# Kernel optimization log

Hardware: AMD Instinct MI355X
Metric: run time of the kernel (lower is better)

## Reference

```python
import jax, jax.numpy as jnp
import numpy as np

L, B, H, R = 128, 4, 768, 97
LN_EPS = 1e-5


def setup_inputs() -> dict:
    key = jax.random.key(0)
    ks = jax.random.split(key, 8)
    s = 0.02
    return {
        "h_re1": jax.random.normal(ks[0], (L, B, H), jnp.float32),
        "h_re2": jax.random.normal(ks[1], (L, B, H), jnp.float32),
        "mask": jax.random.uniform(ks[2], (L, B), jnp.float32),
        "Wr": jax.random.normal(ks[3], (H, 2 * H), jnp.float32) * s,
        "br": jnp.zeros((H,), jnp.float32),
        "Wh": jax.random.normal(ks[4], (H, 3 * H), jnp.float32) * s,
        "bh": jnp.zeros((H,), jnp.float32),
        "gamma": jnp.ones((H,), jnp.float32),
        "beta": jnp.zeros((H,), jnp.float32),
        "Wo": jax.random.normal(ks[5], (R, H), jnp.float32) * s,
        "bo": jnp.zeros((R,), jnp.float32),
    }


def reference(h_re1, h_re2, mask, Wr, br, Wh, bh, gamma, beta, Wo, bo):
    # h_re1, h_re2: [L, B, H]; mask: [L, B]
    h = h_re2.shape[-1]
    # global context: tanh(Linear(cat(h_re1,h_re2))), max over length -> [B, H]
    g = jnp.tanh(jnp.einsum('lbi,hi->lbh', jnp.concatenate([h_re1, h_re2], axis=-1), Wr) + br)
    g = jnp.max(g, axis=0)  # [B, H]
    # hid2hid(cat(r1, r2, g)) == r1 @ W1.T + r2 @ W2.T + g @ W3.T + b
    # (avoids materializing the [L,L,B,3H] repeat+cat tensor)
    W1, W2, W3 = Wh[:, :h], Wh[:, h:2 * h], Wh[:, 2 * h:]
    a = jnp.einsum('lbi,hi->lbh', h_re2, W1)          # varies over first pair axis
    b2 = jnp.einsum('lbi,hi->lbh', h_re2, W2)         # varies over second pair axis
    gp = jnp.einsum('bi,hi->bh', g, W3) + bh          # constant over pairs
    pre = a[:, None, :, :] + b2[None, :, :, :] + gp   # [L, L, B, H]
    # LayerNorm over last dim (biased variance, as in torch)
    mu = jnp.mean(pre, axis=-1, keepdims=True)
    var = jnp.var(pre, axis=-1, keepdims=True)
    x = (pre - mu) * jax.lax.rsqrt(var + LN_EPS) * gamma + beta
    x = jax.nn.elu(x)  # dropout is identity in eval mode
    out = jax.nn.sigmoid(jnp.einsum('klbh,rh->klbr', x, Wo) + bo)  # [L, L, B, R]
    # pairwise mask: mask_e1 * mask_e2, broadcast over relation dim
    m = mask[:, None, :, None] * mask[None, :, :, None]
    return out * m
```

## Files before the change

### kernel.cpp

```cpp
#include <hip/hip_runtime.h>
#include <hip/hip_bf16.h>
#include <stdint.h>

#define L_ 128
#define B_ 4
#define H_ 768
#define R_ 97
#define LN_EPS 1e-5f

typedef _Float16 f16x8 __attribute__((ext_vector_type(8)));
typedef _Float16 f16x4 __attribute__((ext_vector_type(4)));
typedef _Float16 f16x2 __attribute__((ext_vector_type(2)));
typedef float f32x4 __attribute__((ext_vector_type(4)));

extern "C" __device__ _Float16 __ocml_exp2_f16(_Float16);

__device__ inline f16x8 cvt8(float4 v0, float4 v1) {
  f16x8 o;
  o[0] = (_Float16)v0.x; o[1] = (_Float16)v0.y; o[2] = (_Float16)v0.z; o[3] = (_Float16)v0.w;
  o[4] = (_Float16)v1.x; o[5] = (_Float16)v1.y; o[6] = (_Float16)v1.z; o[7] = (_Float16)v1.w;
  return o;
}

__global__ __launch_bounds__(256) void prep_all(const float* __restrict__ h1,
                                                const float* __restrict__ h2,
                                                const float* __restrict__ Wr,
                                                const float* __restrict__ Wh,
                                                const float* __restrict__ Wo,
                                                const float* __restrict__ gamma,
                                                const float* __restrict__ beta,
                                                _Float16* __restrict__ ccH,
                                                _Float16* __restrict__ BpR,
                                                _Float16* __restrict__ BpW,
                                                _Float16* __restrict__ WoP,
                                                _Float16* __restrict__ gbH,
                                                unsigned int* __restrict__ gmaxU) {
  int blk = blockIdx.x;
  if (blk < 512) {
    const float2* s1 = (const float2*)(h1 + (size_t)blk * H_);
    const float2* s2 = (const float2*)(h2 + (size_t)blk * H_);
    f16x2* d = (f16x2*)(ccH + (size_t)blk * (2 * H_));
    for (int i = threadIdx.x; i < H_ / 2; i += 256) {
      float2 v = s1[i]; f16x2 o; o[0] = (_Float16)v.x; o[1] = (_Float16)v.y; d[i] = o;
    }
    for (int i = threadIdx.x; i < H_ / 2; i += 256) {
      float2 v = s2[i]; f16x2 o; o[0] = (_Float16)v.x; o[1] = (_Float16)v.y; d[H_ / 2 + i] = o;
    }
    return;
  }
  blk -= 512;
  if (blk < 576) {
    int c = blk * 256 + threadIdx.x;
    int l = c & 63, u = c >> 6;
    int nt = u % 48, ks = u / 48;
    int n = nt * 16 + (l & 15);
    int k = ks * 32 + ((l >> 4) << 3);
    const float4* s = (const float4*)(Wr + (size_t)n * 1536 + k);
    *(f16x8*)(BpR + (size_t)c * 8) = cvt8(s[0], s[1]);
    return;
  }
  blk -= 576;
  if (blk < 576) {
    int c = blk * 256 + threadIdx.x;
    int l = c & 63, u = c >> 6;
    int nt = u % 96, ks = u / 96;
    int n = nt * 16 + (l & 15);
    int k = ks * 32 + ((l >> 4) << 3);
    const float* src = (n < 768) ? (Wh + (size_t)n * 2304 + k)
                                 : (Wh + (size_t)(n - 768) * 2304 + 768 + k);
    const float4* s = (const float4*)src;
    *(f16x8*)(BpW + (size_t)c * 8) = cvt8(s[0], s[1]);
    return;
  }
  blk -= 576;
  if (blk < 48) {
    int c = blk * 256 + threadIdx.x;
    int l = c & 63, u = c >> 6;
    int nt = u & 7, ks = u >> 3;
    int n = nt * 16 + (l & 15);
    int k = ks * 32 + ((l >> 4) << 3);
    f16x8 o = {};
    if (n < R_) {
      const float4* s = (const float4*)(Wo + (size_t)n * 768 + k);
      o = cvt8(s[0], s[1]);
    }
    *(f16x8*)(WoP + (size_t)c * 8) = o;
    return;
  }
  blk -= 48;
  if (blk < 3) {
    int i = blk * 256 + threadIdx.x;
    if (i < H_) {
      gbH[i] = (_Float16)gamma[i];
      gbH[H_ + i] = (_Float16)beta[i];
    }
    return;
  }
  blk -= 3;
  int i = blk * 256 + threadIdx.x;
  if (i < B_ * H_) gmaxU[i] = 0u;
}

__device__ __forceinline__ void gemm_g_tile(int nb, int mb,
                                            const _Float16* __restrict__ A,
                                            const _Float16* __restrict__ BpR,
                                            const float* __restrict__ br,
                                            unsigned int* __restrict__ gmaxU) {
  int w = threadIdx.x >> 6, l = threadIdx.x & 63;
  int row0 = mb * 32 + (w & 1) * 16;
  int nt0 = nb * 4 + (w >> 1) * 2;
  const f16x8* ap = (const f16x8*)(A + (size_t)(row0 + (l & 15)) * 1536 + (l >> 4) * 8);
  const f16x8* bp = (const f16x8*)(BpR + ((size_t)nt0 * 64 + l) * 8);
  f32x4 acc0 = {}, acc1 = {};
  f16x8 ac = ap[0], b0c = bp[0], b1c = bp[64];
  for (int ks = 0; ks < 48; ++ks) {
    f16x8 an = {}, b0n = {}, b1n = {};
    if (ks < 47) {
      an = ap[(ks + 1) * 4];
      b0n = bp[(size_t)(ks + 1) * 3072];
      b1n = bp[(size_t)(ks + 1) * 3072 + 64];
    }
    acc0 = __builtin_amdgcn_mfma_f32_16x16x32_f16(ac, b0c, acc0, 0, 0, 0);
    acc1 = __builtin_amdgcn_mfma_f32_16x16x32_f16(ac, b1c, acc1, 0, 0, 0);
    ac = an; b0c = b0n; b1c = b1n;
  }
#pragma unroll
  for (int q = 0; q < 2; ++q) {
    f32x4 acc = q ? acc1 : acc0;
    int col = nb * 64 + (w >> 1) * 32 + q * 16 + (l & 15);
#pragma unroll
    for (int r = 0; r < 4; ++r) {
      int row = row0 + (l >> 4) * 4 + r;
      float t = tanhf(acc[r] + br[col]) + 1.0f;
      atomicMax(&gmaxU[(row & 3) * H_ + col], __float_as_uint(t));
    }
  }
}

__device__ __forceinline__ void gemm_ab_tile(int nb, int mb,
                                             const _Float16* __restrict__ ccH,
                                             const _Float16* __restrict__ BpW,
                                             _Float16* __restrict__ aH,
                                             _Float16* __restrict__ bH) {
  int w = threadIdx.x >> 6, l = threadIdx.x & 63;
  int row0 = mb * 32 + (w & 1) * 16;
  int nt0 = nb * 4 + (w >> 1) * 2;
  const f16x8* ap = (const f16x8*)(ccH + (size_t)(row0 + (l & 15)) * 1536 + 768 + (l >> 4) * 8);
  const f16x8* bp = (const f16x8*)(BpW + ((size_t)nt0 * 64 + l) * 8);
  f32x4 acc0 = {}, acc1 = {};
  f16x8 ac = ap[0], b0c = bp[0], b1c = bp[64];
  for (int ks = 0; ks < 24; ++ks) {
    f16x8 an = {}, b0n = {}, b1n = {};
    if (ks < 23) {
      an = ap[(ks + 1) * 4];
      b0n = bp[(size_t)(ks + 1) * 6144];
      b1n = bp[(size_t)(ks + 1) * 6144 + 64];
    }
    acc0 = __builtin_amdgcn_mfma_f32_16x16x32_f16(ac, b0c, acc0, 0, 0, 0);
    acc1 = __builtin_amdgcn_mfma_f32_16x16x32_f16(ac, b1c, acc1, 0, 0, 0);
    ac = an; b0c = b0n; b1c = b1n;
  }
#pragma unroll
  for (int q = 0; q < 2; ++q) {
    f32x4 acc = q ? acc1 : acc0;
    int col = nb * 64 + (w >> 1) * 32 + q * 16 + (l & 15);
#pragma unroll
    for (int r = 0; r < 4; ++r) {
      int row = row0 + (l >> 4) * 4 + r;
      float v = acc[r];
      if (col < 768) aH[(size_t)row * H_ + col] = (_Float16)v;
      else           bH[(size_t)row * H_ + (col - 768)] = (_Float16)v;
    }
  }
}

__global__ __launch_bounds__(256) void gemm_both(const _Float16* __restrict__ ccH,
                                                 const _Float16* __restrict__ BpR,
                                                 const _Float16* __restrict__ BpW,
                                                 const float* __restrict__ br,
                                                 unsigned int* __restrict__ gmaxU,
                                                 _Float16* __restrict__ aH,
                                                 _Float16* __restrict__ bH) {
  int bid = blockIdx.x;
  if (bid < 192) {
    gemm_g_tile(bid % 12, bid / 12, ccH, BpR, br, gmaxU);
  } else {
    int j2 = bid - 192;
    gemm_ab_tile(j2 % 24, j2 / 24, ccH, BpW, aH, bH);
  }
}

__global__ __launch_bounds__(256) void gp_kernel(const float* __restrict__ Wh,
                                                 const unsigned int* __restrict__ gmaxU,
                                                 const float* __restrict__ bh,
                                                 float* __restrict__ gpv) {
  int n = blockIdx.x;
  int w = threadIdx.x >> 6, l = threadIdx.x & 63;
  const float* wr = Wh + (size_t)n * 2304 + 1536;
  const unsigned int* gm = gmaxU + (size_t)w * H_;
  float s = 0.f;
#pragma unroll
  for (int t = 0; t < 12; ++t) {
    int i = l + 64 * t;
    s += wr[i] * (__uint_as_float(gm[i]) - 1.0f);
  }
#pragma unroll
  for (int off = 32; off; off >>= 1) s += __shfl_xor(s, off);
  if (l == 0) gpv[(size_t)w * H_ + n] = s + bh[n];
}

__global__ __launch_bounds__(256) void stats(const _Float16* __restrict__ aH,
                                             const _Float16* __restrict__ bH,
                                             const float* __restrict__ gpv,
                                             _Float16* __restrict__ aH2,
                                             float* __restrict__ S,
                                             float* __restrict__ Q) {
  int r = blockIdx.x * 4 + (threadIdx.x >> 6);
  int l = threadIdx.x & 63;
  float s = 0.f, q = 0.f;
  if (r < 512) {
    int b = r & 3;
    const f16x4* ap = (const f16x4*)(aH + (size_t)r * H_);
    const float4* gp4 = (const float4*)(gpv + (size_t)b * H_);
    f16x4* op = (f16x4*)(aH2 + (size_t)r * H_);
#pragma unroll
    for (int t = 0; t < 3; ++t) {
      int i = t * 64 + l;
      f16x4 av = ap[i];
      float4 g4 = gp4[i];
      f16x4 o;
      o[0] = (_Float16)((float)av[0] + g4.x);
      o[1] = (_Float16)((float)av[1] + g4.y);
      o[2] = (_Float16)((float)av[2] + g4.z);
      o[3] = (_Float16)((float)av[3] + g4.w);
      op[i] = o;
#pragma unroll
      for (int j = 0; j < 4; ++j) { float y = (float)o[j]; s += y; q += y * y; }
    }
  } else {
    const f16x4* bp = (const f16x4*)(bH + (size_t)(r - 512) * H_);
#pragma unroll
    for (int t = 0; t < 3; ++t) {
      f16x4 bv = bp[t * 64 + l];
#pragma unroll
      for (int j = 0; j < 4; ++j) { float y = (float)bv[j]; s += y; q += y * y; }
    }
  }
#pragma unroll
  for (int off = 32; off; off >>= 1) {
    s += __shfl_xor(s, off);
    q += __shfl_xor(q, off);
  }
  if (l == 0) { S[r] = s; Q[r] = q; }
}

__global__ __launch_bounds__(256) void dotab(const _Float16* __restrict__ aH2,
                                             const _Float16* __restrict__ bH,
                                             const float* __restrict__ S,
                                             const float* __restrict__ Q,
                                             float* __restrict__ mu_arr,
                                             float* __restrict__ rs_arr) {
  int w = threadIdx.x >> 6, l = threadIdx.x & 63;
  int ltq = blockIdx.x, kt = blockIdx.y, b = blockIdx.z;
  int lt = ltq * 4 + w;
  const f16x8* ap = (const f16x8*)(aH2 + ((size_t)(kt * 16 + (l & 15)) * 4 + b) * H_ + (l >> 4) * 8);
  const f16x8* bp = (const f16x8*)(bH + ((size_t)(lt * 16 + (l & 15)) * 4 + b) * H_ + (l >> 4) * 8);
  f32x4 acc = {};
  f16x8 a0 = ap[0], b0 = bp[0], a1 = ap[4], b1 = bp[4];
  for (int ks = 0; ks < 24; ++ks) {
    f16x8 a2 = {}, b2 = {};
    if (ks < 22) { a2 = ap[(ks + 2) * 4]; b2 = bp[(ks + 2) * 4]; }
    acc = __builtin_amdgcn_mfma_f32_16x16x32_f16(a0, b0, acc, 0, 0, 0);
    a0 = a1; b0 = b1; a1 = a2; b1 = b2;
  }
#pragma unroll
  for (int r = 0; r < 4; ++r) {
    int k = kt * 16 + (l >> 4) * 4 + r;
    int lg = lt * 16 + (l & 15);
    int arow = k * 4 + b, brow = lg * 4 + b;
    float mu = (S[arow] + S[512 + brow]) * (1.f / H_);
    float q2 = Q[arow] + Q[512 + brow] + 2.f * acc[r];
    float var = fmaxf(q2 * (1.f / H_) - mu * mu, 0.f);
    float rs = rsqrtf(var + LN_EPS);
    size_t idx = (size_t)k * 512 + (size_t)lg * 4 + b;
    mu_arr[idx] = mu;
    rs_arr[idx] = rs;
  }
}

__global__ __launch_bounds__(256) void fused2(const _Float16* __restrict__ aH2,
                                              const _Float16* __restrict__ bH,
                                              const _Float16* __restrict__ gbH,
                                              const _Float16* __restrict__ WoP,
                                              const float* __restrict__ bo,
                                              const float* __restrict__ mask,
                                              const float* __restrict__ mu_arr,
                                              const float* __restrict__ rs_arr,
                                              float* __restrict__ out) {
  __shared__ __align__(16) _Float16 WoLds[3][4096];
  int tid = threadIdx.x, w = tid >> 6, l = tid & 63;
  int m0 = blockIdx.x * 64;
  int myrow = m0 + w * 16 + (l & 15);
  int b = myrow & 3, li = (myrow >> 2) & 127, kk = myrow >> 9;
  const f16x8* ap = (const f16x8*)(aH2 + ((size_t)kk * 4 + b) * H_ + (l >> 4) * 8);
  const f16x8* bp = (const f16x8*)(bH + ((size_t)li * 4 + b) * H_ + (l >> 4) * 8);
  const f16x8* gp8 = (const f16x8*)(gbH + (l >> 4) * 8);
  const f16x8* be8 = (const f16x8*)(gbH + H_ + (l >> 4) * 8);
  float mu = mu_arr[myrow], rs = rs_arr[myrow];
  _Float16 muh = (_Float16)mu, rsh = (_Float16)rs;
  _Float16 l2e = (_Float16)1.44269504f;
  f16x8 mu8, rs8, zero8, one8, l2e8;
#pragma unroll
  for (int j = 0; j < 8; ++j) {
    mu8[j] = muh; rs8[j] = rsh;
    zero8[j] = (_Float16)0.f; one8[j] = (_Float16)1.f; l2e8[j] = l2e;
  }

  const uint4* wog = (const uint4*)WoP;
  {
    uint4* d0 = (uint4*)&WoLds[0][0];
    uint4* d1 = (uint4*)&WoLds[1][0];
    d0[tid] = wog[tid];            d0[256 + tid] = wog[256 + tid];
    d1[tid] = wog[512 + tid];      d1[256 + tid] = wog[512 + 256 + tid];
  }
  __syncthreads();

  f16x8 a8 = ap[0], b8 = bp[0], g8 = gp8[0], e8 = be8[0];

  int cur = 0, wt = 2;
  f32x4 acc[7] = {};
  for (int ks = 0; ks < 24; ++ks) {
    uint4 wo0 = {}, wo1 = {};
    f16x8 an = {}, bn = {}, gn = {}, en = {};
    if (ks < 22) {
      wo0 = wog[(ks + 2) * 512 + tid];
      wo1 = wog[(ks + 2) * 512 + 256 + tid];
    }
    if (ks < 23) {
      an = ap[(ks + 1) * 4];
      bn = bp[(ks + 1) * 4];
      gn = gp8[(ks + 1) * 4];
      en = be8[(ks + 1) * 4];
    }
    f16x8 x = a8 + b8;
    f16x8 c1 = rs8 * g8;
    f16x8 yv = (x - mu8) * c1 + e8;
    f16x8 y2 = yv * l2e8;
    f16x8 ex;
#pragma unroll
    for (int j = 0; j < 8; ++j) ex[j] = __ocml_exp2_f16(y2[j]);
    ex = ex - one8;
    f16x8 av = __builtin_elementwise_max(yv, zero8) + __builtin_elementwise_min(ex, zero8);
    __syncthreads();
    if (ks < 22) {
      uint4* d = (uint4*)&WoLds[wt][0];
      d[tid] = wo0;
      d[256 + tid] = wo1;
    }
    const f16x8* bvp = (const f16x8*)&WoLds[cur][0];
#pragma unroll
    for (int q = 0; q < 7; ++q) {
      f16x8 bv = bvp[q * 64 + l];
      acc[q] = __builtin_amdgcn_mfma_f32_16x16x32_f16(av, bv, acc[q], 0, 0, 0);
    }
    a8 = an; b8 = bn; g8 = gn; e8 = en;
    cur = (cur == 2) ? 0 : cur + 1;
    wt = (wt == 2) ? 0 : wt + 1;
  }
  float mv[4];
#pragma unroll
  for (int r = 0; r < 4; ++r) {
    int row = m0 + w * 16 + (l >> 4) * 4 + r;
    int bb = row & 3, ll = (row >> 2) & 127, kx = row >> 9;
    mv[r] = mask[kx * 4 + bb] * mask[ll * 4 + bb];
  }
#pragma unroll
  for (int q = 0; q < 7; ++q) {
    int col = q * 16 + (l & 15);
    if (col < R_) {
      float bov = bo[col];
#pragma unroll
      for (int r = 0; r < 4; ++r) {
        int row = m0 + w * 16 + (l >> 4) * 4 + r;
        float z = acc[q][r] + bov;
        out[(size_t)row * R_ + col] = mv[r] / (1.f + __expf(-z));
      }
    }
  }
}

extern "C" void kernel_launch(void* const* d_in, const int* in_sizes, int n_in,
                              void* d_out, int out_size, void* d_ws, size_t ws_size,
                              hipStream_t stream) {
  const float* h1    = (const float*)d_in[0];
  const float* h2    = (const float*)d_in[1];
  const float* mask  = (const float*)d_in[2];
  const float* Wr    = (const float*)d_in[3];
  const float* br    = (const float*)d_in[4];
  const float* Wh    = (const float*)d_in[5];
  const float* bh    = (const float*)d_in[6];
  const float* gamma = (const float*)d_in[7];
  const float* beta  = (const float*)d_in[8];
  const float* Wo    = (const float*)d_in[9];
  const float* bo    = (const float*)d_in[10];
  float* out = (float*)d_out;
  char* ws = (char*)d_ws;

  _Float16* ccH = (_Float16*)ws;                    size_t off = 512 * 1536 * 2;
  _Float16* BpR = (_Float16*)(ws + off);            off += (size_t)1536 * 768 * 2;
  _Float16* BpW = (_Float16*)(ws + off);            off += (size_t)768 * 1536 * 2;
  _Float16* WoP = (_Float16*)(ws + off);            off += 768 * 128 * 2;
  _Float16* gbH = (_Float16*)(ws + off);            off += 4096;
  _Float16* aH  = (_Float16*)(ws + off);            off += 512 * 768 * 2;
  _Float16* bH  = (_Float16*)(ws + off);            off += 512 * 768 * 2;
  _Float16* aH2 = (_Float16*)(ws + off);            off += 512 * 768 * 2;
  unsigned int* gmaxU = (unsigned int*)(ws + off);  off += 3072 * 4;
  float* gpv = (float*)(ws + off);                  off += 3072 * 4;
  float* S   = (float*)(ws + off);                  off += 1024 * 4;
  float* Q   = (float*)(ws + off);                  off += 1024 * 4;
  float* mu_arr = (float*)(ws + off);               off += 65536 * 4;
  float* rs_arr = (float*)(ws + off);               off += 65536 * 4;

  prep_all<<<512 + 576 + 576 + 48 + 3 + 12, 256, 0, stream>>>(h1, h2, Wr, Wh, Wo, gamma, beta,
                                                              ccH, BpR, BpW, WoP, gbH, gmaxU);

  gemm_both<<<576, 256, 0, stream>>>(ccH, BpR, BpW, br, gmaxU, aH, bH);
  gp_kernel<<<768, 256, 0, stream>>>(Wh, gmaxU, bh, gpv);
  stats<<<256, 256, 0, stream>>>(aH, bH, gpv, aH2, S, Q);
  dotab<<<dim3(2, 8, 4), 256, 0, stream>>>(aH2, bH, S, Q, mu_arr, rs_arr);

  fused2<<<1024, 256, 0, stream>>>(aH2, bH, gbH, WoP, bo, mask, mu_arr, rs_arr, out);
}
```

Measured before the change: 92.51 us.

## Fuse fp32-to-fp16 input conversion into GEMM loads and restage Wo tiles in LDS

The GEMMs now read fp32 h1/h2/Wr/Wh directly and convert them to fp16 in registers, so the separate pre-pass that wrote converted and packed copies of those tensors (and its workspace traffic) is gone. This trades a write and reread of about 5 MB of fp16 for reading fp32 operands inside the GEMM, where the loads are now strided rows rather than the old packed layout. The fused2 kernel also changes from a 3-slot rotating Wo prefetch to three phases that each bulk-load 8 k-steps of Wo into a larger shared buffer. That adds barriers and removes the overlap between loads and compute.

Result: slower. 142.8 us (+54.4%).

```diff
diff --git a/kernel.cpp b/kernel.cpp
--- a/kernel.cpp
+++ b/kernel.cpp
@@ -22,57 +22,13 @@
   return o;
 }
 
-__global__ __launch_bounds__(256) void prep_all(const float* __restrict__ h1,
-                                                const float* __restrict__ h2,
-                                                const float* __restrict__ Wr,
-                                                const float* __restrict__ Wh,
-                                                const float* __restrict__ Wo,
+__global__ __launch_bounds__(256) void prep_all(const float* __restrict__ Wo,
                                                 const float* __restrict__ gamma,
                                                 const float* __restrict__ beta,
-                                                _Float16* __restrict__ ccH,
-                                                _Float16* __restrict__ BpR,
-                                                _Float16* __restrict__ BpW,
                                                 _Float16* __restrict__ WoP,
                                                 _Float16* __restrict__ gbH,
                                                 unsigned int* __restrict__ gmaxU) {
   int blk = blockIdx.x;
-  if (blk < 512) {
-    const float2* s1 = (const float2*)(h1 + (size_t)blk * H_);
-    const float2* s2 = (const float2*)(h2 + (size_t)blk * H_);
-    f16x2* d = (f16x2*)(ccH + (size_t)blk * (2 * H_));
-    for (int i = threadIdx.x; i < H_ / 2; i += 256) {
-      float2 v = s1[i]; f16x2 o; o[0] = (_Float16)v.x; o[1] = (_Float16)v.y; d[i] = o;
-    }
-    for (int i = threadIdx.x; i < H_ / 2; i += 256) {
-      float2 v = s2[i]; f16x2 o; o[0] = (_Float16)v.x; o[1] = (_Float16)v.y; d[H_ / 2 + i] = o;
-    }
-    return;
-  }
-  blk -= 512;
-  if (blk < 576) {
-    int c = blk * 256 + threadIdx.x;
-    int l = c & 63, u = c >> 6;
-    int nt = u % 48, ks = u / 48;
-    int n = nt * 16 + (l & 15);
-    int k = ks * 32 + ((l >> 4) << 3);
-    const float4* s = (const float4*)(Wr + (size_t)n * 1536 + k);
-    *(f16x8*)(BpR + (size_t)c * 8) = cvt8(s[0], s[1]);
-    return;
-  }
-  blk -= 576;
-  if (blk < 576) {
-    int c = blk * 256 + threadIdx.x;
-    int l = c & 63, u = c >> 6;
-    int nt = u % 96, ks = u / 96;
-    int n = nt * 16 + (l & 15);
-    int k = ks * 32 + ((l >> 4) << 3);
-    const float* src = (n < 768) ? (Wh + (size_t)n * 2304 + k)
-                                 : (Wh + (size_t)(n - 768) * 2304 + 768 + k);
-    const float4* s = (const float4*)src;
-    *(f16x8*)(BpW + (size_t)c * 8) = cvt8(s[0], s[1]);
-    return;
-  }
-  blk -= 576;
   if (blk < 48) {
     int c = blk * 256 + threadIdx.x;
     int l = c & 63, u = c >> 6;
@@ -102,91 +58,99 @@
 }
 
 __device__ __forceinline__ void gemm_g_tile(int nb, int mb,
-                                            const _Float16* __restrict__ A,
-                                            const _Float16* __restrict__ BpR,
+                                            const float* __restrict__ h1,
+                                            const float* __restrict__ h2,
+                                            const float* __restrict__ Wr,
                                             const float* __restrict__ br,
                                             unsigned int* __restrict__ gmaxU) {
   int w = threadIdx.x >> 6, l = threadIdx.x & 63;
   int row0 = mb * 32 + (w & 1) * 16;
   int nt0 = nb * 4 + (w >> 1) * 2;
-  const f16x8* ap = (const f16x8*)(A + (size_t)(row0 + (l & 15)) * 1536 + (l >> 4) * 8);
-  const f16x8* bp = (const f16x8*)(BpR + ((size_t)nt0 * 64 + l) * 8);
+  int r = row0 + (l & 15);
+  int kbase = (l >> 4) * 8;
+  const float4* a1p = (const float4*)(h1 + (size_t)r * H_ + kbase);
+  const float4* a2p = (const float4*)(h2 + (size_t)r * H_ + kbase);
+  const float4* b0p = (const float4*)(Wr + (size_t)(nt0 * 16 + (l & 15)) * 1536 + kbase);
+  const float4* b1p = (const float4*)(Wr + (size_t)((nt0 + 1) * 16 + (l & 15)) * 1536 + kbase);
   f32x4 acc0 = {}, acc1 = {};
-  f16x8 ac = ap[0], b0c = bp[0], b1c = bp[64];
+#pragma unroll 4
   for (int ks = 0; ks < 48; ++ks) {
-    f16x8 an = {}, b0n = {}, b1n = {};
-    if (ks < 47) {
-      an = ap[(ks + 1) * 4];
-      b0n = bp[(size_t)(ks + 1) * 3072];
-      b1n = bp[(size_t)(ks + 1) * 3072 + 64];
-    }
-    acc0 = __builtin_amdgcn_mfma_f32_16x16x32_f16(ac, b0c, acc0, 0, 0, 0);
-    acc1 = __builtin_amdgcn_mfma_f32_16x16x32_f16(ac, b1c, acc1, 0, 0, 0);
-    ac = an; b0c = b0n; b1c = b1n;
+    const float4* asrc = (ks < 24) ? (a1p + ks * 8) : (a2p + (ks - 24) * 8);
+    f16x8 av = cvt8(asrc[0], asrc[1]);
+    f16x8 b0 = cvt8(b0p[ks * 8], b0p[ks * 8 + 1]);
+    f16x8 b1 = cvt8(b1p[ks * 8], b1p[ks * 8 + 1]);
+    acc0 = __builtin_amdgcn_mfma_f32_16x16x32_f16(av, b0, acc0, 0, 0, 0);
+    acc1 = __builtin_amdgcn_mfma_f32_16x16x32_f16(av, b1, acc1, 0, 0, 0);
   }
 #pragma unroll
   for (int q = 0; q < 2; ++q) {
     f32x4 acc = q ? acc1 : acc0;
-    int col = nb * 64 + (w >> 1) * 32 + q * 16 + (l & 15);
-#pragma unroll
-    for (int r = 0; r < 4; ++r) {
-      int row = row0 + (l >> 4) * 4 + r;
-      float t = tanhf(acc[r] + br[col]) + 1.0f;
+    int col = (nt0 + q) * 16 + (l & 15);
+#pragma unroll
+    for (int rr = 0; rr < 4; ++rr) {
+      int row = row0 + (l >> 4) * 4 + rr;
+      float t = tanhf(acc[rr] + br[col]) + 1.0f;
       atomicMax(&gmaxU[(row & 3) * H_ + col], __float_as_uint(t));
     }
   }
 }
 
 __device__ __forceinline__ void gemm_ab_tile(int nb, int mb,
-                                             const _Float16* __restrict__ ccH,
-                                             const _Float16* __restrict__ BpW,
+                                             const float* __restrict__ h2,
+                                             const float* __restrict__ Wh,
                                              _Float16* __restrict__ aH,
                                              _Float16* __restrict__ bH) {
   int w = threadIdx.x >> 6, l = threadIdx.x & 63;
   int row0 = mb * 32 + (w & 1) * 16;
   int nt0 = nb * 4 + (w >> 1) * 2;
-  const f16x8* ap = (const f16x8*)(ccH + (size_t)(row0 + (l & 15)) * 1536 + 768 + (l >> 4) * 8);
-  const f16x8* bp = (const f16x8*)(BpW + ((size_t)nt0 * 64 + l) * 8);
+  int r = row0 + (l & 15);
+  int kbase = (l >> 4) * 8;
+  const float4* ap = (const float4*)(h2 + (size_t)r * H_ + kbase);
+  int n0 = nt0 * 16 + (l & 15);
+  int n1 = n0 + 16;
+  const float* b0s = (n0 < 768) ? (Wh + (size_t)n0 * 2304 + kbase)
+                                : (Wh + (size_t)(n0 - 768) * 2304 + 768 + kbase);
+  const float* b1s = (n1 < 768) ? (Wh + (size_t)n1 * 2304 + kbase)
+                                : (Wh + (size_t)(n1 - 768) * 2304 + 768 + kbase);
+  const float4* b0p = (const float4*)b0s;
+  const float4* b1p = (const float4*)b1s;
   f32x4 acc0 = {}, acc1 = {};
-  f16x8 ac = ap[0], b0c = bp[0], b1c = bp[64];
+#pragma unroll 4
   for (int ks = 0; ks < 24; ++ks) {
-    f16x8 an = {}, b0n = {}, b1n = {};
-    if (ks < 23) {
-      an = ap[(ks + 1) * 4];
-      b0n = bp[(size_t)(ks + 1) * 6144];
-      b1n = bp[(size_t)(ks + 1) * 6144 + 64];
-    }
-    acc0 = __builtin_amdgcn_mfma_f32_16x16x32_f16(ac, b0c, acc0, 0, 0, 0);
-    acc1 = __builtin_amdgcn_mfma_f32_16x16x32_f16(ac, b1c, acc1, 0, 0, 0);
-    ac = an; b0c = b0n; b1c = b1n;
+    f16x8 av = cvt8(ap[ks * 8], ap[ks * 8 + 1]);
+    f16x8 b0 = cvt8(b0p[ks * 8], b0p[ks * 8 + 1]);
+    f16x8 b1 = cvt8(b1p[ks * 8], b1p[ks * 8 + 1]);
+    acc0 = __builtin_amdgcn_mfma_f32_16x16x32_f16(av, b0, acc0, 0, 0, 0);
+    acc1 = __builtin_amdgcn_mfma_f32_16x16x32_f16(av, b1, acc1, 0, 0, 0);
   }
 #pragma unroll
   for (int q = 0; q < 2; ++q) {
     f32x4 acc = q ? acc1 : acc0;
-    int col = nb * 64 + (w >> 1) * 32 + q * 16 + (l & 15);
-#pragma unroll
-    for (int r = 0; r < 4; ++r) {
-      int row = row0 + (l >> 4) * 4 + r;
-      float v = acc[r];
+    int col = (nt0 + q) * 16 + (l & 15);
+#pragma unroll
+    for (int rr = 0; rr < 4; ++rr) {
+      int row = row0 + (l >> 4) * 4 + rr;
+      float v = acc[rr];
       if (col < 768) aH[(size_t)row * H_ + col] = (_Float16)v;
       else           bH[(size_t)row * H_ + (col - 768)] = (_Float16)v;
     }
   }
 }
 
-__global__ __launch_bounds__(256) void gemm_both(const _Float16* __restrict__ ccH,
-                                                 const _Float16* __restrict__ BpR,
-                                                 const _Float16* __restrict__ BpW,
+__global__ __launch_bounds__(256) void gemm_both(const float* __restrict__ h1,
+                                                 const float* __restrict__ h2,
+                                                 const float* __restrict__ Wr,
+                                                 const float* __restrict__ Wh,
                                                  const float* __restrict__ br,
                                                  unsigned int* __restrict__ gmaxU,
                                                  _Float16* __restrict__ aH,
                                                  _Float16* __restrict__ bH) {
   int bid = blockIdx.x;
   if (bid < 192) {
-    gemm_g_tile(bid % 12, bid / 12, ccH, BpR, br, gmaxU);
+    gemm_g_tile(bid % 12, bid / 12, h1, h2, Wr, br, gmaxU);
   } else {
     int j2 = bid - 192;
-    gemm_ab_tile(j2 % 24, j2 / 24, ccH, BpW, aH, bH);
+    gemm_ab_tile(j2 % 24, j2 / 24, h2, Wh, aH, bH);
   }
 }
 
@@ -297,7 +261,7 @@
                                               const float* __restrict__ mu_arr,
                                               const float* __restrict__ rs_arr,
                                               float* __restrict__ out) {
-  __shared__ __align__(16) _Float16 WoLds[3][4096];
+  __shared__ __align__(16) uint4 WoLds[4096];
   int tid = threadIdx.x, w = tid >> 6, l = tid & 63;
   int m0 = blockIdx.x * 64;
   int myrow = m0 + w * 16 + (l & 15);
@@ -317,55 +281,51 @@
   }
 
   const uint4* wog = (const uint4*)WoP;
-  {
-    uint4* d0 = (uint4*)&WoLds[0][0];
-    uint4* d1 = (uint4*)&WoLds[1][0];
-    d0[tid] = wog[tid];            d0[256 + tid] = wog[256 + tid];
-    d1[tid] = wog[512 + tid];      d1[256 + tid] = wog[512 + 256 + tid];
-  }
-  __syncthreads();
-
   f16x8 a8 = ap[0], b8 = bp[0], g8 = gp8[0], e8 = be8[0];
 
-  int cur = 0, wt = 2;
   f32x4 acc[7] = {};
-  for (int ks = 0; ks < 24; ++ks) {
-    uint4 wo0 = {}, wo1 = {};
-    f16x8 an = {}, bn = {}, gn = {}, en = {};
-    if (ks < 22) {
-      wo0 = wog[(ks + 2) * 512 + tid];
-      wo1 = wog[(ks + 2) * 512 + 256 + tid];
-    }
-    if (ks < 23) {
-      an = ap[(ks + 1) * 4];
-      bn = bp[(ks + 1) * 4];
-      gn = gp8[(ks + 1) * 4];
-      en = be8[(ks + 1) * 4];
-    }
-    f16x8 x = a8 + b8;
-    f16x8 c1 = rs8 * g8;
-    f16x8 yv = (x - mu8) * c1 + e8;
-    f16x8 y2 = yv * l2e8;
-    f16x8 ex;
-#pragma unroll
-    for (int j = 0; j < 8; ++j) ex[j] = __ocml_exp2_f16(y2[j]);
-    ex = ex - one8;
-    f16x8 av = __builtin_elementwise_max(yv, zero8) + __builtin_elementwise_min(ex, zero8);
+  for (int ph = 0; ph < 3; ++ph) {
     __syncthreads();
-    if (ks < 22) {
-      uint4* d = (uint4*)&WoLds[wt][0];
-      d[tid] = wo0;
-      d[256 + tid] = wo1;
-    }
-    const f16x8* bvp = (const f16x8*)&WoLds[cur][0];
-#pragma unroll
-    for (int q = 0; q < 7; ++q) {
-      f16x8 bv = bvp[q * 64 + l];
-      acc[q] = __builtin_amdgcn_mfma_f32_16x16x32_f16(av, bv, acc[q], 0, 0, 0);
-    }
-    a8 = an; b8 = bn; g8 = gn; e8 = en;
-    cur = (cur == 2) ? 0 : cur + 1;
-    wt = (wt == 2) ? 0 : wt + 1;
+    const uint4* gsrc = wog + (size_t)ph * 4096;
+#pragma unroll
+    for (int g = 0; g < 4; ++g) {
+      uint4 v0 = gsrc[(g * 4 + 0) * 256 + tid];
+      uint4 v1 = gsrc[(g * 4 + 1) * 256 + tid];
+      uint4 v2 = gsrc[(g * 4 + 2) * 256 + tid];
+      uint4 v3 = gsrc[(g * 4 + 3) * 256 + tid];
+      WoLds[(g * 4 + 0) * 256 + tid] = v0;
+      WoLds[(g * 4 + 1) * 256 + tid] = v1;
+      WoLds[(g * 4 + 2) * 256 + tid] = v2;
+      WoLds[(g * 4 + 3) * 256 + tid] = v3;
+    }
+    __syncthreads();
+#pragma unroll
+    for (int s = 0; s < 8; ++s) {
+      int ks = ph * 8 + s;
+      f16x8 an = {}, bn = {}, gn = {}, en = {};
+      if (ks < 23) {
+        an = ap[(ks + 1) * 4];
+        bn = bp[(ks + 1) * 4];
+        gn = gp8[(ks + 1) * 4];
+        en = be8[(ks + 1) * 4];
+      }
+      f16x8 x = a8 + b8;
+      f16x8 c1 = rs8 * g8;
+      f16x8 yv = (x - mu8) * c1 + e8;
+      f16x8 y2 = yv * l2e8;
+      f16x8 ex;
+#pragma unroll
+      for (int j = 0; j < 8; ++j) ex[j] = __ocml_exp2_f16(y2[j]);
+      ex = ex - one8;
+      f16x8 av = __builtin_elementwise_max(yv, zero8) + __builtin_elementwise_min(ex, zero8);
+      const f16x8* bvp = (const f16x8*)&WoLds[s * 512];
+#pragma unroll
+      for (int q = 0; q < 7; ++q) {
+        f16x8 bv = bvp[q * 64 + l];
+        acc[q] = __builtin_amdgcn_mfma_f32_16x16x32_f16(av, bv, acc[q], 0, 0, 0);
+      }
+      a8 = an; b8 = bn; g8 = gn; e8 = en;
+    }
   }
   float mv[4];
 #pragma unroll
@@ -406,10 +366,7 @@
   float* out = (float*)d_out;
   char* ws = (char*)d_ws;
 
-  _Float16* ccH = (_Float16*)ws;                    size_t off = 512 * 1536 * 2;
-  _Float16* BpR = (_Float16*)(ws + off);            off += (size_t)1536 * 768 * 2;
-  _Float16* BpW = (_Float16*)(ws + off);            off += (size_t)768 * 1536 * 2;
-  _Float16* WoP = (_Float16*)(ws + off);            off += 768 * 128 * 2;
+  _Float16* WoP = (_Float16*)ws;                    size_t off = 768 * 128 * 2;
   _Float16* gbH = (_Float16*)(ws + off);            off += 4096;
   _Float16* aH  = (_Float16*)(ws + off);            off += 512 * 768 * 2;
   _Float16* bH  = (_Float16*)(ws + off);            off += 512 * 768 * 2;
@@ -421,10 +378,9 @@
   float* mu_arr = (float*)(ws + off);               off += 65536 * 4;
   float* rs_arr = (float*)(ws + off);               off += 65536 * 4;
 
-  prep_all<<<512 + 576 + 576 + 48 + 3 + 12, 256, 0, stream>>>(h1, h2, Wr, Wh, Wo, gamma, beta,
-                                                              ccH, BpR, BpW, WoP, gbH, gmaxU);
-
-  gemm_both<<<576, 256, 0, stream>>>(ccH, BpR, BpW, br, gmaxU, aH, bH);
+  prep_all<<<48 + 3 + 12, 256, 0, stream>>>(Wo, gamma, beta, WoP, gbH, gmaxU);
+
+  gemm_both<<<576, 256, 0, stream>>>(h1, h2, Wr, Wh, br, gmaxU, aH, bH);
   gp_kernel<<<768, 256, 0, stream>>>(Wh, gmaxU, bh, gpv);
   stats<<<256, 256, 0, stream>>>(aH, bH, gpv, aH2, S, Q);
   dotab<<<dim3(2, 8, 4), 256, 0, stream>>>(aH2, bH, S, Q, mu_arr, rs_arr);
```

## Stage Wo in four-step LDS chunks instead of triple-buffered per-step pipeline

Applied to the files above, without the earlier changes.

Replaces the three-slot rotating LDS buffer for the output projection weights, which issued one barrier and prefetch per K step, with six phases. Each phase loads four K steps of weights into LDS between two barriers, then runs four MFMA steps from that chunk. This cuts barriers per block from 24 to 12 and batches global loads. The cost is that weight loads no longer overlap with compute, so each phase stalls on global latency.

Result: no change. 92.12 us (-0.4%).

```diff
diff --git a/kernel.cpp b/kernel.cpp
--- a/kernel.cpp
+++ b/kernel.cpp
@@ -297,7 +297,7 @@
                                               const float* __restrict__ mu_arr,
                                               const float* __restrict__ rs_arr,
                                               float* __restrict__ out) {
-  __shared__ __align__(16) _Float16 WoLds[3][4096];
+  __shared__ __align__(16) uint4 WoLds[2048];
   int tid = threadIdx.x, w = tid >> 6, l = tid & 63;
   int m0 = blockIdx.x * 64;
   int myrow = m0 + w * 16 + (l & 15);
@@ -317,55 +317,51 @@
   }
 
   const uint4* wog = (const uint4*)WoP;
-  {
-    uint4* d0 = (uint4*)&WoLds[0][0];
-    uint4* d1 = (uint4*)&WoLds[1][0];
-    d0[tid] = wog[tid];            d0[256 + tid] = wog[256 + tid];
-    d1[tid] = wog[512 + tid];      d1[256 + tid] = wog[512 + 256 + tid];
-  }
-  __syncthreads();
-
   f16x8 a8 = ap[0], b8 = bp[0], g8 = gp8[0], e8 = be8[0];
 
-  int cur = 0, wt = 2;
   f32x4 acc[7] = {};
-  for (int ks = 0; ks < 24; ++ks) {
-    uint4 wo0 = {}, wo1 = {};
-    f16x8 an = {}, bn = {}, gn = {}, en = {};
-    if (ks < 22) {
-      wo0 = wog[(ks + 2) * 512 + tid];
-      wo1 = wog[(ks + 2) * 512 + 256 + tid];
-    }
-    if (ks < 23) {
-      an = ap[(ks + 1) * 4];
-      bn = bp[(ks + 1) * 4];
-      gn = gp8[(ks + 1) * 4];
-      en = be8[(ks + 1) * 4];
-    }
-    f16x8 x = a8 + b8;
-    f16x8 c1 = rs8 * g8;
-    f16x8 yv = (x - mu8) * c1 + e8;
-    f16x8 y2 = yv * l2e8;
-    f16x8 ex;
-#pragma unroll
-    for (int j = 0; j < 8; ++j) ex[j] = __ocml_exp2_f16(y2[j]);
-    ex = ex - one8;
-    f16x8 av = __builtin_elementwise_max(yv, zero8) + __builtin_elementwise_min(ex, zero8);
+  for (int ph = 0; ph < 6; ++ph) {
     __syncthreads();
-    if (ks < 22) {
-      uint4* d = (uint4*)&WoLds[wt][0];
-      d[tid] = wo0;
-      d[256 + tid] = wo1;
-    }
-    const f16x8* bvp = (const f16x8*)&WoLds[cur][0];
-#pragma unroll
-    for (int q = 0; q < 7; ++q) {
-      f16x8 bv = bvp[q * 64 + l];
-      acc[q] = __builtin_amdgcn_mfma_f32_16x16x32_f16(av, bv, acc[q], 0, 0, 0);
-    }
-    a8 = an; b8 = bn; g8 = gn; e8 = en;
-    cur = (cur == 2) ? 0 : cur + 1;
-    wt = (wt == 2) ? 0 : wt + 1;
+    const uint4* gsrc = wog + (size_t)ph * 2048;
+#pragma unroll
+    for (int g = 0; g < 2; ++g) {
+      uint4 v0 = gsrc[(g * 4 + 0) * 256 + tid];
+      uint4 v1 = gsrc[(g * 4 + 1) * 256 + tid];
+      uint4 v2 = gsrc[(g * 4 + 2) * 256 + tid];
+      uint4 v3 = gsrc[(g * 4 + 3) * 256 + tid];
+      WoLds[(g * 4 + 0) * 256 + tid] = v0;
+      WoLds[(g * 4 + 1) * 256 + tid] = v1;
+      WoLds[(g * 4 + 2) * 256 + tid] = v2;
+      WoLds[(g * 4 + 3) * 256 + tid] = v3;
+    }
+    __syncthreads();
+#pragma unroll
+    for (int s = 0; s < 4; ++s) {
+      int ks = ph * 4 + s;
+      f16x8 an = {}, bn = {}, gn = {}, en = {};
+      if (ks < 23) {
+        an = ap[(ks + 1) * 4];
+        bn = bp[(ks + 1) * 4];
+        gn = gp8[(ks + 1) * 4];
+        en = be8[(ks + 1) * 4];
+      }
+      f16x8 x = a8 + b8;
+      f16x8 c1 = rs8 * g8;
+      f16x8 yv = (x - mu8) * c1 + e8;
+      f16x8 y2 = yv * l2e8;
+      f16x8 ex;
+#pragma unroll
+      for (int j = 0; j < 8; ++j) ex[j] = __ocml_exp2_f16(y2[j]);
+      ex = ex - one8;
+      f16x8 av = __builtin_elementwise_max(yv, zero8) + __builtin_elementwise_min(ex, zero8);
+      const f16x8* bvp = (const f16x8*)&WoLds[s * 512];
+#pragma unroll
+      for (int q = 0; q < 7; ++q) {
+        f16x8 bv = bvp[q * 64 + l];
+        acc[q] = __builtin_amdgcn_mfma_f32_16x16x32_f16(av, bv, acc[q], 0, 0, 0);
+      }
+      a8 = an; b8 = bn; g8 = gn; e8 = en;
+    }
   }
   float mv[4];
 #pragma unroll
```
